# Optimization experiments

Measured on AMD Instinct MI355X. Metric: run time of the kernel, lower is better.

## Reference

```python
import jax, jax.numpy as jnp
import numpy as np


def setup_inputs() -> dict:
    key = jax.random.key(0)
    x = jax.random.normal(key, (16, 512, 512, 8), dtype=jnp.float32)
    # 3x3 structuring element with center False: neighbors-only local max
    mask = jnp.array([[True, True, True],
                      [True, False, True],
                      [True, True, True]])
    return {"x": x, "mask": mask}


def reference(x, mask):
    # Equivalent of tf.nn.dilation2d(x, where(mask, 0, -inf), SAME, stride 1):
    # masked_max[b,i,j,c] = max over (di,dj) in mask of x[b,i+di-ph, j+dj-pw, c]
    # (out-of-bounds treated as -inf, matching dilation's identity padding).
    kh, kw = mask.shape  # small static window (e.g. 3x3)
    H, W = x.shape[1], x.shape[2]
    ph, pw = (kh - 1) // 2, (kw - 1) // 2
    neg_inf = jnp.asarray(-jnp.inf, x.dtype)
    xp = jnp.pad(x, ((0, 0), (ph, kh - 1 - ph), (pw, kw - 1 - pw), (0, 0)),
                 constant_values=-np.inf)
    masked_max = jnp.full_like(x, -np.inf)
    for di in range(kh):          # fixed small kernel loop (9 taps), not a data-dim loop
        for dj in range(kw):
            win = xp[:, di:di + H, dj:dj + W, :]
            masked_max = jnp.maximum(masked_max, jnp.where(mask[di, dj], win, neg_inf))
    # suppressed = cast(x > masked_max) * x
    return (x > masked_max).astype(x.dtype) * x
```

## Files before the change

kernel.cpp:

```cpp
#include <hip/hip_runtime.h>
#include <math.h>


constexpr int Hdim = 512;
constexpr int Wdim = 512;
constexpr int ROW  = Wdim * 2;
constexpr int TH   = 8;
constexpr int TW   = 64;
constexpr int LROWS = TH + 2;
constexpr int LCOLS = TW * 2 + 4;

typedef float floatx4 __attribute__((ext_vector_type(4)));

__device__ __forceinline__ float4 f4max(float4 a, float4 b) {
    return make_float4(fmaxf(a.x,b.x), fmaxf(a.y,b.y), fmaxf(a.z,b.z), fmaxf(a.w,b.w));
}

__device__ __forceinline__ void nt_store_f4(float4* p, float4 v) {
    floatx4 nv;
    nv.x = v.x; nv.y = v.y; nv.z = v.z; nv.w = v.w;
    __builtin_nontemporal_store(nv, reinterpret_cast<floatx4*>(p));
}

__global__ __launch_bounds__(256, 7) void nms_kernel(
    const float4* __restrict__ x,
    const unsigned char* __restrict__ mask_bytes,
    float4* __restrict__ out)
{
    __shared__ float4 lds[LROWS][LCOLS];

    const int* mi = (const int*)mask_bytes;
    bool intlay = true;
    #pragma unroll
    for (int i = 0; i < 9; ++i) { int v = mi[i]; intlay = intlay && (v == 0 || v == 1); }
    bool m[9];
    #pragma unroll
    for (int i = 0; i < 9; ++i) m[i] = intlay ? (mi[i] != 0) : (mask_bytes[i] != 0);

    const float4 NEG = make_float4(-INFINITY, -INFINITY, -INFINITY, -INFINITY);

    int b  = blockIdx.x;
    int wg = b & 7;
    int hg = (b >> 3) & 63;
    int n  = b >> 9;
    int h0 = hg * TH;
    int w0 = wg * TW;
    int t  = threadIdx.x;

    int gb = ((n * Hdim + (h0 - 1)) * Wdim + w0) * 2;
    #pragma unroll
    for (int i = 0; i < 5; ++i) {
        int idx = t + i * 256;
        int r = idx >> 7;
        int c = idx & 127;
        int h = h0 - 1 + r;
        float4 v = NEG;
        if (h >= 0 && h < Hdim)
            v = x[gb + r * ROW + c];
        lds[r][2 + c] = v;
    }
    if (t < 40) {
        int r    = t >> 2;
        int q    = t & 3;
        int side = q >> 1;
        int c4   = q & 1;
        int h    = h0 - 1 + r;
        int wgl  = side ? (w0 + TW) : (w0 - 1);
        float4 v = NEG;
        if (h >= 0 && h < Hdim && wgl >= 0 && wgl < Wdim)
            v = x[((n * Hdim + h) * Wdim + wgl) * 2 + c4];
        lds[r][side ? (2 + 2 * TW + c4) : c4] = v;
    }
    __syncthreads();

    int cidx = t & 127;
    int hb   = (t >> 7) * 4;
    int col  = 2 + cidx;
    int obase = ((n * Hdim + h0) * Wdim + w0) * 2 + cidx;

    float4 R0a = NEG, R0b = NEG, R1b = NEG, CTb = NEG;
    #pragma unroll
    for (int k = 0; k < 6; ++k) {
        int r = hb + k;
        float4 a  = lds[r][col - 2];
        float4 bb = lds[r][col];
        float4 cc = lds[r][col + 2];

        float4 R0 = NEG, R1 = NEG, R2 = NEG;
        if (m[0]) R0 = f4max(R0, a);
        if (m[1]) R0 = f4max(R0, bb);
        if (m[2]) R0 = f4max(R0, cc);
        if (m[3]) R1 = f4max(R1, a);
        if (m[4]) R1 = f4max(R1, bb);
        if (m[5]) R1 = f4max(R1, cc);
        if (m[6]) R2 = f4max(R2, a);
        if (m[7]) R2 = f4max(R2, bb);
        if (m[8]) R2 = f4max(R2, cc);

        if (k >= 2) {
            float4 mm  = f4max(f4max(R0a, R1b), R2);
            float4 ctr = CTb;
            float4 o;
            o.x = (ctr.x > mm.x) ? ctr.x : 0.0f;
            o.y = (ctr.y > mm.y) ? ctr.y : 0.0f;
            o.z = (ctr.z > mm.z) ? ctr.z : 0.0f;
            o.w = (ctr.w > mm.w) ? ctr.w : 0.0f;
            nt_store_f4(&out[obase + (hb + k - 2) * ROW], o);
        }
        R0a = R0b; R0b = R0; R1b = R1; CTb = bb;
    }
}

extern "C" void kernel_launch(void* const* d_in, const int* in_sizes, int n_in,
                              void* d_out, int out_size, void* d_ws, size_t ws_size,
                              hipStream_t stream) {
    const float4* x = (const float4*)d_in[0];
    const unsigned char* mask = (const unsigned char*)d_in[1];
    float4* out = (float4*)d_out;

    int grid = 16 * (Hdim / TH) * (Wdim / TW);
    int block = 256;
    nms_kernel<<<grid, block, 0, stream>>>(x, mask, out);
}
```

Baseline: 234.9 us.

## Stream full-width row strips through a rotating LDS ring buffer with prefetch

Each block now owns a full 512-pixel-wide strip of 16 rows, and 1024 threads each handle one float4 column. Rows are staged through a 4-slot LDS ring while the next row is prefetched from global memory. This removes the horizontal halo loads and most of the vertical halo re-reads. The cost is a __syncthreads per row, a grid of only 512 blocks of 1024 threads, and boundary handling done by clamping the row index and forcing values to -inf.

```diff
diff --git a/kernel.cpp b/kernel.cpp
--- a/kernel.cpp
+++ b/kernel.cpp
@@ -2,13 +2,11 @@
 #include <math.h>
 
 
-constexpr int Hdim = 512;
-constexpr int Wdim = 512;
-constexpr int ROW  = Wdim * 2;
-constexpr int TH   = 8;
-constexpr int TW   = 64;
-constexpr int LROWS = TH + 2;
-constexpr int LCOLS = TW * 2 + 4;
+constexpr int Hdim  = 512;
+constexpr int Wdim  = 512;
+constexpr int ROWF4 = Wdim * 2;
+constexpr int TH    = 16;
+constexpr int NSLOT = 4;
 
 typedef float floatx4 __attribute__((ext_vector_type(4)));
 
@@ -17,17 +15,16 @@
 }
 
 __device__ __forceinline__ void nt_store_f4(float4* p, float4 v) {
-    floatx4 nv;
-    nv.x = v.x; nv.y = v.y; nv.z = v.z; nv.w = v.w;
+    floatx4 nv; nv.x = v.x; nv.y = v.y; nv.z = v.z; nv.w = v.w;
     __builtin_nontemporal_store(nv, reinterpret_cast<floatx4*>(p));
 }
 
-__global__ __launch_bounds__(256, 7) void nms_kernel(
+__global__ __launch_bounds__(1024, 8) void nms_kernel(
     const float4* __restrict__ x,
     const unsigned char* __restrict__ mask_bytes,
     float4* __restrict__ out)
 {
-    __shared__ float4 lds[LROWS][LCOLS];
+    __shared__ float4 L[NSLOT][ROWF4];
 
     const int* mi = (const int*)mask_bytes;
     bool intlay = true;
@@ -40,64 +37,64 @@
     const float4 NEG = make_float4(-INFINITY, -INFINITY, -INFINITY, -INFINITY);
 
     int b  = blockIdx.x;
-    int wg = b & 7;
-    int hg = (b >> 3) & 63;
-    int n  = b >> 9;
+    int hg = b & 31;
+    int n  = b >> 5;
     int h0 = hg * TH;
-    int w0 = wg * TW;
     int t  = threadIdx.x;
+    bool topb = (hg == 0);
+    bool botb = (hg == 31);
 
-    int gb = ((n * Hdim + (h0 - 1)) * Wdim + w0) * 2;
-    #pragma unroll
-    for (int i = 0; i < 5; ++i) {
-        int idx = t + i * 256;
-        int r = idx >> 7;
-        int c = idx & 127;
-        int h = h0 - 1 + r;
-        float4 v = NEG;
-        if (h >= 0 && h < Hdim)
-            v = x[gb + r * ROW + c];
-        lds[r][2 + c] = v;
-    }
-    if (t < 40) {
-        int r    = t >> 2;
-        int q    = t & 3;
-        int side = q >> 1;
-        int c4   = q & 1;
-        int h    = h0 - 1 + r;
-        int wgl  = side ? (w0 + TW) : (w0 - 1);
-        float4 v = NEG;
-        if (h >= 0 && h < Hdim && wgl >= 0 && wgl < Wdim)
-            v = x[((n * Hdim + h) * Wdim + wgl) * 2 + c4];
-        lds[r][side ? (2 + 2 * TW + c4) : c4] = v;
+    bool aok = (t >= 2);
+    bool cok = (t <= ROWF4 - 3);
+    int ia = aok ? t - 2 : t;
+    int ic = cok ? t + 2 : t;
+
+    int xbase = n * Hdim * ROWF4;
+
+    {
+        int r0 = topb ? 0 : h0 - 1;
+        float4 v0 = x[xbase + r0 * ROWF4 + t];
+        float4 v1 = x[xbase + h0 * ROWF4 + t];
+        float4 v2 = x[xbase + (h0 + 1) * ROWF4 + t];
+        L[0][t] = v0; L[1][t] = v1; L[2][t] = v2;
     }
     __syncthreads();
 
-    int cidx = t & 127;
-    int hb   = (t >> 7) * 4;
-    int col  = 2 + cidx;
-    int obase = ((n * Hdim + h0) * Wdim + w0) * 2 + cidx;
+    float4 R0a = NEG, R0b = NEG, R1b = NEG, CTb = NEG;
 
-    float4 R0a = NEG, R0b = NEG, R1b = NEG, CTb = NEG;
     #pragma unroll
-    for (int k = 0; k < 6; ++k) {
-        int r = hb + k;
-        float4 a  = lds[r][col - 2];
-        float4 bb = lds[r][col];
-        float4 cc = lds[r][col + 2];
+    for (int r = 0; r < TH + 2; ++r) {
+        float4 pf;
+        const bool doPf = (r <= TH - 2);
+        if (doPf) {
+            int hp = h0 + 2 + r;
+            if (hp > Hdim - 1) hp = Hdim - 1;
+            pf = x[xbase + hp * ROWF4 + t];
+        }
+
+        const int s = r & 3;
+        float4 a  = L[s][ia];
+        float4 bb = L[s][t];
+        float4 c  = L[s][ic];
+        a.x = aok ? a.x : -INFINITY; a.y = aok ? a.y : -INFINITY;
+        a.z = aok ? a.z : -INFINITY; a.w = aok ? a.w : -INFINITY;
+        c.x = cok ? c.x : -INFINITY; c.y = cok ? c.y : -INFINITY;
+        c.z = cok ? c.z : -INFINITY; c.w = cok ? c.w : -INFINITY;
 
         float4 R0 = NEG, R1 = NEG, R2 = NEG;
         if (m[0]) R0 = f4max(R0, a);
         if (m[1]) R0 = f4max(R0, bb);
-        if (m[2]) R0 = f4max(R0, cc);
+        if (m[2]) R0 = f4max(R0, c);
         if (m[3]) R1 = f4max(R1, a);
         if (m[4]) R1 = f4max(R1, bb);
-        if (m[5]) R1 = f4max(R1, cc);
+        if (m[5]) R1 = f4max(R1, c);
         if (m[6]) R2 = f4max(R2, a);
         if (m[7]) R2 = f4max(R2, bb);
-        if (m[8]) R2 = f4max(R2, cc);
+        if (m[8]) R2 = f4max(R2, c);
+        if (r == 0 && topb)      R0 = NEG;
+        if (r == TH + 1 && botb) R2 = NEG;
 
-        if (k >= 2) {
+        if (r >= 2) {
             float4 mm  = f4max(f4max(R0a, R1b), R2);
             float4 ctr = CTb;
             float4 o;
@@ -105,9 +102,13 @@
             o.y = (ctr.y > mm.y) ? ctr.y : 0.0f;
             o.z = (ctr.z > mm.z) ? ctr.z : 0.0f;
             o.w = (ctr.w > mm.w) ? ctr.w : 0.0f;
-            nt_store_f4(&out[obase + (hb + k - 2) * ROW], o);
+            nt_store_f4(&out[xbase + (h0 + r - 2) * ROWF4 + t], o);
         }
+
         R0a = R0b; R0b = R0; R1b = R1; CTb = bb;
+
+        if (doPf) L[(r + 3) & 3][t] = pf;
+        __syncthreads();
     }
 }
 
@@ -118,7 +119,7 @@
     const unsigned char* mask = (const unsigned char*)d_in[1];
     float4* out = (float4*)d_out;
 
-    int grid = 16 * (Hdim / TH) * (Wdim / TW);
-    int block = 256;
+    int grid = 16 * (Hdim / TH);
+    int block = 1024;
     nms_kernel<<<grid, block, 0, stream>>>(x, mask, out);
 }
```

After: 238.0 us. No clear change (+1.3%).
